# Optimization experiments

Measured on AMD Instinct MI355X. Metric: run time of the kernel, lower is better.

## Reference

```python
import jax, jax.numpy as jnp
import numpy as np

N_QUBITS = 7
N_LAYERS = 2
HILBERT = 2 ** N_QUBITS


def _rx(t):
    c = jnp.cos(t / 2).astype(jnp.complex64)
    s = (-1j * jnp.sin(t / 2)).astype(jnp.complex64)
    return jnp.stack([jnp.stack([c, s]), jnp.stack([s, c])])


def _ry(t):
    c = jnp.cos(t / 2).astype(jnp.complex64)
    s = jnp.sin(t / 2).astype(jnp.complex64)
    return jnp.stack([jnp.stack([c, -s]), jnp.stack([s, c])])


def _rz(t):
    z0 = jnp.exp(-0.5j * t).astype(jnp.complex64)
    z1 = jnp.exp(0.5j * t).astype(jnp.complex64)
    zero = jnp.zeros_like(z0)
    return jnp.stack([jnp.stack([z0, zero]), jnp.stack([zero, z1])])


def _apply_1q(state, U, q):
    # state: [B, 2, 2, ..., 2]; wire q lives on axis q+1 (wire 0 = MSB, PennyLane convention)
    ax = q + 1
    out = jnp.tensordot(U, state, axes=[[1], [ax]])  # new gate axis at 0
    return jnp.moveaxis(out, 0, ax)


def _apply_cnot(state, c, t):
    c_ax, t_ax = c + 1, t + 1
    s0 = jax.lax.index_in_dim(state, 0, c_ax, keepdims=False)
    s1 = jax.lax.index_in_dim(state, 1, c_ax, keepdims=False)
    t2 = t_ax - 1 if t_ax > c_ax else t_ax  # target axis after control axis removed
    s1 = jnp.flip(s1, axis=t2)  # X on target within control=1 block
    return jnp.stack([s0, s1], axis=c_ax)


def setup_inputs() -> dict:
    key = jax.random.key(0)
    k1, k2 = jax.random.split(key)
    x = jax.random.normal(k1, (131072, HILBERT), dtype=jnp.float32)
    weights = jax.random.uniform(k2, (N_LAYERS, N_QUBITS, 3), dtype=jnp.float32) * (2 * np.pi)
    return {"x": x, "weights": weights}


def reference(x, weights):
    B = x.shape[0]
    norms = jnp.maximum(jnp.linalg.norm(x, axis=-1, keepdims=True), 1e-8)
    psi = (x / norms).astype(jnp.complex64)
    state = psi.reshape((B,) + (2,) * N_QUBITS)
    for layer in range(N_LAYERS):
        for q in range(N_QUBITS):
            state = _apply_1q(state, _rx(weights[layer, q, 0]), q)
            state = _apply_1q(state, _ry(weights[layer, q, 1]), q)
            state = _apply_1q(state, _rz(weights[layer, q, 2]), q)
        for q in range(N_QUBITS):
            state = _apply_cnot(state, q, (q + 1) % N_QUBITS)
    probs = jnp.abs(state) ** 2  # real [B, 2,...,2]
    zs = []
    for q in range(N_QUBITS):
        other = tuple(a for a in range(1, N_QUBITS + 1) if a != q + 1)
        p = probs.sum(axis=other)  # [B, 2] marginal of wire q
        zs.append(p[:, 0] - p[:, 1])
    return jnp.stack(zs, axis=-1)  # [B, N_QUBITS]
```

## Files before the change

kernel.cpp:

```cpp
#include <hip/hip_runtime.h>
#include <hip/hip_bf16.h>


typedef __attribute__((ext_vector_type(8)))  short short8;
typedef __attribute__((ext_vector_type(16))) float f32x16;

static __device__ __forceinline__ short f2bf(float f) {
  __bf16 h = (__bf16)f;
  return __builtin_bit_cast(short, h);
}

static __device__ __forceinline__ int widx(int P, int s, int k) {
  return ((((P << 2) + (s >> 5)) * 8 + (k >> 4)) * 64 +
          ((s & 31) + ((k >> 3) & 1) * 32)) * 8 + (k & 7);
}

__global__ void qnn_build_w(const float* __restrict__ wts,
                            short* __restrict__ W) {
  const int k = blockIdx.x;
  const int l = threadIdx.x;

  float c0r = (2 * l     == k) ? 1.f : 0.f, c0i = 0.f;
  float c1r = (2 * l + 1 == k) ? 1.f : 0.f, c1i = 0.f;

  for (int layer = 0; layer < 2; ++layer) {
    for (int q = 0; q < 7; ++q) {
      const float t0 = 0.5f * wts[(layer * 7 + q) * 3 + 0];
      const float t1 = 0.5f * wts[(layer * 7 + q) * 3 + 1];
      const float t2 = 0.5f * wts[(layer * 7 + q) * 3 + 2];
      const float cx = __cosf(t0), sx = __sinf(t0);
      const float cy = __cosf(t1), sy = __sinf(t1);
      const float cz = __cosf(t2), sz = __sinf(t2);
      const float m00r =  cy * cx, m00i =  sy * sx;
      const float m01r = -sy * cx, m01i = -cy * sx;
      const float m10r =  sy * cx, m10i = -cy * sx;
      const float m11r =  cy * cx, m11i = -sy * sx;
      const float g00r = m00r * cz + m00i * sz, g00i = m00i * cz - m00r * sz;
      const float g01r = m01r * cz + m01i * sz, g01i = m01i * cz - m01r * sz;
      const float g10r = m10r * cz - m10i * sz, g10i = m10i * cz + m10r * sz;
      const float g11r = m11r * cz - m11i * sz, g11i = m11i * cz + m11r * sz;

      const int b = 6 - q;
      if (b == 0) {
        const float n0r = g00r*c0r - g00i*c0i + g01r*c1r - g01i*c1i;
        const float n0i = g00r*c0i + g00i*c0r + g01r*c1i + g01i*c1r;
        const float n1r = g10r*c0r - g10i*c0i + g11r*c1r - g11i*c1i;
        const float n1i = g10r*c0i + g10i*c0r + g11r*c1i + g11i*c1r;
        c0r = n0r; c0i = n0i; c1r = n1r; c1i = n1i;
      } else {
        const int xm  = 1 << (b - 1);
        const int myb = (l >> (b - 1)) & 1;
        const float p0r = __shfl_xor(c0r, xm), p0i = __shfl_xor(c0i, xm);
        const float p1r = __shfl_xor(c1r, xm), p1i = __shfl_xor(c1i, xm);
        const float gar = myb ? g11r : g00r, gai = myb ? g11i : g00i;
        const float gbr = myb ? g10r : g01r, gbi = myb ? g10i : g01i;
        const float n0r = gar*c0r - gai*c0i + gbr*p0r - gbi*p0i;
        const float n0i = gar*c0i + gai*c0r + gbr*p0i + gbi*p0r;
        const float n1r = gar*c1r - gai*c1i + gbr*p1r - gbi*p1i;
        const float n1i = gar*c1i + gai*c1r + gbr*p1i + gbi*p1r;
        c0r = n0r; c0i = n0i; c1r = n1r; c1i = n1i;
      }
    }
    #pragma unroll
    for (int q = 0; q < 7; ++q) {
      const int bc = 6 - q;
      const int bt = 6 - ((q + 1) % 7);
      if (bt == 0) {
        if (l & 1) { float tr=c0r, ti=c0i; c0r=c1r; c0i=c1i; c1r=tr; c1i=ti; }
      } else if (bc == 0) {
        c1r = __shfl_xor(c1r, 32);
        c1i = __shfl_xor(c1i, 32);
      } else {
        const int xm = 1 << (bt - 1);
        const float p0r = __shfl_xor(c0r, xm), p0i = __shfl_xor(c0i, xm);
        const float p1r = __shfl_xor(c1r, xm), p1i = __shfl_xor(c1i, xm);
        if ((l >> (bc - 1)) & 1) { c0r=p0r; c0i=p0i; c1r=p1r; c1i=p1i; }
      }
    }
  }

  W[widx(0, 2 * l,     k)] = f2bf(c0r);
  W[widx(0, 2 * l + 1, k)] = f2bf(c1r);
  W[widx(1, 2 * l,     k)] = f2bf(c0i);
  W[widx(1, 2 * l + 1, k)] = f2bf(c1i);
}

__global__ __launch_bounds__(256, 4) void qnn_main(
    const float* __restrict__ x, const short* __restrict__ W,
    float* __restrict__ out) {
  const int tid = threadIdx.x;
  const int l   = tid & 63;
  const int wv  = tid >> 6;
  const int col = l & 31;
  const int h   = l >> 5;

  __shared__ short8 xb[512];
  __shared__ float  red[4][32][7];

  const int t0 = blockIdx.x;

  float4 fa[2], fb[2];
  #pragma unroll
  for (int i = 0; i < 2; ++i) {
    const int p = i * 256 + tid;
    const int r = p >> 4, q = p & 15;
    const float* gp = x + (size_t)(t0 * 32 + r) * 128 + q * 8;
    fa[i] = *reinterpret_cast<const float4*>(gp);
    fb[i] = *reinterpret_cast<const float4*>(gp + 4);
  }

  short8 A0[8], A1[8];
  #pragma unroll
  for (int j = 0; j < 8; ++j) {
    const int off = ((wv * 8 + j) * 64 + l) * 8;
    A0[j] = *reinterpret_cast<const short8*>(W + off);
    A1[j] = *reinterpret_cast<const short8*>(W + 16384 + off);
  }

  #pragma unroll
  for (int i = 0; i < 2; ++i) {
    const int p = i * 256 + tid;
    const int r = p >> 4, q = p & 15;
    short8 c;
    c[0]=f2bf(fa[i].x); c[1]=f2bf(fa[i].y); c[2]=f2bf(fa[i].z); c[3]=f2bf(fa[i].w);
    c[4]=f2bf(fb[i].x); c[5]=f2bf(fb[i].y); c[6]=f2bf(fb[i].z); c[7]=f2bf(fb[i].w);
    xb[r * 16 + (q ^ (r & 7))] = c;
  }
  asm volatile("s_waitcnt lgkmcnt(0)" ::: "memory");
  __builtin_amdgcn_s_barrier();
  asm volatile("" ::: "memory");

  f32x16 acc0 = {0.f,0.f,0.f,0.f,0.f,0.f,0.f,0.f,
                 0.f,0.f,0.f,0.f,0.f,0.f,0.f,0.f};
  f32x16 acc1 = {0.f,0.f,0.f,0.f,0.f,0.f,0.f,0.f,
                 0.f,0.f,0.f,0.f,0.f,0.f,0.f,0.f};
  #pragma unroll
  for (int j = 0; j < 8; ++j) {
    const int q = j * 2 + h;
    const short8 bfr = xb[col * 16 + (q ^ (col & 7))];
    acc0 = __builtin_amdgcn_mfma_f32_32x32x16_bf16(A0[j], bfr, acc0, 0, 0, 0);
    acc1 = __builtin_amdgcn_mfma_f32_32x32x16_bf16(A1[j], bfr, acc1, 0, 0, 0);
  }

  {
    float aS[8], aD[8];
    #pragma unroll
    for (int i = 0; i < 8; ++i) {
      const float pe = acc0[2*i]   * acc0[2*i]   + acc1[2*i]   * acc1[2*i];
      const float po = acc0[2*i+1] * acc0[2*i+1] + acc1[2*i+1] * acc1[2*i+1];
      aS[i] = pe + po;
      aD[i] = pe - po;
    }
    float bS[4], bD[4];
    #pragma unroll
    for (int i = 0; i < 4; ++i) {
      bS[i] = aS[2*i] + aS[2*i+1];
      bD[i] = aS[2*i] - aS[2*i+1];
    }
    float u0 = ((aD[0]+aD[1]) + (aD[2]+aD[3])) + ((aD[4]+aD[5]) + (aD[6]+aD[7]));
    float u1 = (bD[0] + bD[1]) + (bD[2] + bD[3]);
    const float cS0 = bS[0] + bS[1], cD0 = bS[0] - bS[1];
    const float cS1 = bS[2] + bS[3], cD1 = bS[2] - bS[3];
    float u3 = cD0 + cD1;
    float u4 = cS0 - cS1;
    float T  = cS0 + cS1;

    const float Tp = __shfl_xor(T, 32);
    const float u2 = h ? (Tp - T) : (T - Tp);
    T += Tp;
    u0 += __shfl_xor(u0, 32);
    u1 += __shfl_xor(u1, 32);
    u3 += __shfl_xor(u3, 32);
    u4 += __shfl_xor(u4, 32);

    if (h == 0) {
      red[wv][col][0] = T;
      red[wv][col][1] = u0;
      red[wv][col][2] = u1;
      red[wv][col][3] = u2;
      red[wv][col][4] = u3;
      red[wv][col][5] = u4;
    }
  }

  asm volatile("s_waitcnt lgkmcnt(0)" ::: "memory");
  __builtin_amdgcn_s_barrier();
  asm volatile("" ::: "memory");

  if (tid < 32) {
    const int c = tid;
    const float T0 = red[0][c][0], T1 = red[1][c][0];
    const float T2 = red[2][c][0], T3 = red[3][c][0];
    const float sT  = (T0 + T1) + (T2 + T3);
    const float inv = 1.0f / sT;
    const float z0 = (T0 + T1) - (T2 + T3);
    const float z1 = (T0 - T1) + (T2 - T3);
    float zr[5];
    #pragma unroll
    for (int i = 0; i < 5; ++i)
      zr[i] = (red[0][c][5-i] + red[1][c][5-i]) +
              (red[2][c][5-i] + red[3][c][5-i]);
    float* o = out + (size_t)(t0 * 32 + c) * 7;
    o[0] = z0 * inv; o[1] = z1 * inv; o[2] = zr[0] * inv; o[3] = zr[1] * inv;
    o[4] = zr[2] * inv; o[5] = zr[3] * inv; o[6] = zr[4] * inv;
  }
}

extern "C" void kernel_launch(void* const* d_in, const int* in_sizes, int n_in,
                              void* d_out, int out_size, void* d_ws, size_t ws_size,
                              hipStream_t stream) {
  const float* x   = (const float*)d_in[0];
  const float* wts = (const float*)d_in[1];
  float* out = (float*)d_out;
  short* W   = (short*)d_ws;

  const int B     = in_sizes[0] / 128;
  const int grid  = B / 32;

  qnn_build_w<<<128, 64, 0, stream>>>(wts, W);
  qnn_main<<<grid, 256, 0, stream>>>(x, W, out);
}
```

Measured before the change: 25.55 us.

## Process two 32-row tiles per block with double-buffered LDS staging

Each block now handles 64 batch rows as two 32-row halves, so the W fragment loads into registers are amortised over twice as many rows. Global loads for the second half are issued before the first half's MFMA compute and staged into a second LDS buffer afterwards, overlapping memory latency with compute. The grid halves, which reduces parallelism and adds a barrier per stage, and the larger LDS footprint and live registers may lower occupancy.

```diff
diff --git a/kernel.cpp b/kernel.cpp
--- a/kernel.cpp
+++ b/kernel.cpp
@@ -94,20 +94,11 @@
   const int col = l & 31;
   const int h   = l >> 5;
 
-  __shared__ short8 xb[512];
-  __shared__ float  red[4][32][7];
+  __shared__ short8 xb[2][512];
+  __shared__ float  red[4][64][6];
 
   const int t0 = blockIdx.x;
-
-  float4 fa[2], fb[2];
-  #pragma unroll
-  for (int i = 0; i < 2; ++i) {
-    const int p = i * 256 + tid;
-    const int r = p >> 4, q = p & 15;
-    const float* gp = x + (size_t)(t0 * 32 + r) * 128 + q * 8;
-    fa[i] = *reinterpret_cast<const float4*>(gp);
-    fb[i] = *reinterpret_cast<const float4*>(gp + 4);
-  }
+  const float* xbase = x + (size_t)t0 * 64 * 128;
 
   short8 A0[8], A1[8];
   #pragma unroll
@@ -117,32 +108,41 @@
     A1[j] = *reinterpret_cast<const short8*>(W + 16384 + off);
   }
 
-  #pragma unroll
-  for (int i = 0; i < 2; ++i) {
-    const int p = i * 256 + tid;
-    const int r = p >> 4, q = p & 15;
-    short8 c;
-    c[0]=f2bf(fa[i].x); c[1]=f2bf(fa[i].y); c[2]=f2bf(fa[i].z); c[3]=f2bf(fa[i].w);
-    c[4]=f2bf(fb[i].x); c[5]=f2bf(fb[i].y); c[6]=f2bf(fb[i].z); c[7]=f2bf(fb[i].w);
-    xb[r * 16 + (q ^ (r & 7))] = c;
-  }
-  asm volatile("s_waitcnt lgkmcnt(0)" ::: "memory");
-  __builtin_amdgcn_s_barrier();
-  asm volatile("" ::: "memory");
-
-  f32x16 acc0 = {0.f,0.f,0.f,0.f,0.f,0.f,0.f,0.f,
-                 0.f,0.f,0.f,0.f,0.f,0.f,0.f,0.f};
-  f32x16 acc1 = {0.f,0.f,0.f,0.f,0.f,0.f,0.f,0.f,
-                 0.f,0.f,0.f,0.f,0.f,0.f,0.f,0.f};
-  #pragma unroll
-  for (int j = 0; j < 8; ++j) {
-    const int q = j * 2 + h;
-    const short8 bfr = xb[col * 16 + (q ^ (col & 7))];
-    acc0 = __builtin_amdgcn_mfma_f32_32x32x16_bf16(A0[j], bfr, acc0, 0, 0, 0);
-    acc1 = __builtin_amdgcn_mfma_f32_32x32x16_bf16(A1[j], bfr, acc1, 0, 0, 0);
-  }
-
-  {
+  float4 fa[2], fb[2];
+
+  auto LOAD = [&](int H) {
+    #pragma unroll
+    for (int i = 0; i < 2; ++i) {
+      const int p = i * 256 + tid;
+      const int r = p >> 4, q = p & 15;
+      const float* gp = xbase + (size_t)(H * 32 + r) * 128 + q * 8;
+      fa[i] = *reinterpret_cast<const float4*>(gp);
+      fb[i] = *reinterpret_cast<const float4*>(gp + 4);
+    }
+  };
+  auto STAGE = [&](int H) {
+    #pragma unroll
+    for (int i = 0; i < 2; ++i) {
+      const int p = i * 256 + tid;
+      const int r = p >> 4, q = p & 15;
+      short8 c;
+      c[0]=f2bf(fa[i].x); c[1]=f2bf(fa[i].y); c[2]=f2bf(fa[i].z); c[3]=f2bf(fa[i].w);
+      c[4]=f2bf(fb[i].x); c[5]=f2bf(fb[i].y); c[6]=f2bf(fb[i].z); c[7]=f2bf(fb[i].w);
+      xb[H][r * 16 + (q ^ (r & 7))] = c;
+    }
+  };
+  auto COMPUTE = [&](int H) {
+    f32x16 acc0 = {0.f,0.f,0.f,0.f,0.f,0.f,0.f,0.f,
+                   0.f,0.f,0.f,0.f,0.f,0.f,0.f,0.f};
+    f32x16 acc1 = {0.f,0.f,0.f,0.f,0.f,0.f,0.f,0.f,
+                   0.f,0.f,0.f,0.f,0.f,0.f,0.f,0.f};
+    #pragma unroll
+    for (int j = 0; j < 8; ++j) {
+      const int q = j * 2 + h;
+      const short8 bfr = xb[H][col * 16 + (q ^ (col & 7))];
+      acc0 = __builtin_amdgcn_mfma_f32_32x32x16_bf16(A0[j], bfr, acc0, 0, 0, 0);
+      acc1 = __builtin_amdgcn_mfma_f32_32x32x16_bf16(A1[j], bfr, acc1, 0, 0, 0);
+    }
     float aS[8], aD[8];
     #pragma unroll
     for (int i = 0; i < 8; ++i) {
@@ -174,20 +174,36 @@
     u4 += __shfl_xor(u4, 32);
 
     if (h == 0) {
-      red[wv][col][0] = T;
-      red[wv][col][1] = u0;
-      red[wv][col][2] = u1;
-      red[wv][col][3] = u2;
-      red[wv][col][4] = u3;
-      red[wv][col][5] = u4;
-    }
-  }
-
+      const int row = H * 32 + col;
+      red[wv][row][0] = T;
+      red[wv][row][1] = u0;
+      red[wv][row][2] = u1;
+      red[wv][row][3] = u2;
+      red[wv][row][4] = u3;
+      red[wv][row][5] = u4;
+    }
+  };
+
+  LOAD(0);
+  STAGE(0);
+  LOAD(1);
+  asm volatile("" ::: "memory");
   asm volatile("s_waitcnt lgkmcnt(0)" ::: "memory");
   __builtin_amdgcn_s_barrier();
   asm volatile("" ::: "memory");
 
-  if (tid < 32) {
+  COMPUTE(0);
+  STAGE(1);
+  asm volatile("s_waitcnt lgkmcnt(0)" ::: "memory");
+  __builtin_amdgcn_s_barrier();
+  asm volatile("" ::: "memory");
+
+  COMPUTE(1);
+  asm volatile("s_waitcnt lgkmcnt(0)" ::: "memory");
+  __builtin_amdgcn_s_barrier();
+  asm volatile("" ::: "memory");
+
+  if (tid < 64) {
     const int c = tid;
     const float T0 = red[0][c][0], T1 = red[1][c][0];
     const float T2 = red[2][c][0], T3 = red[3][c][0];
@@ -200,7 +216,7 @@
     for (int i = 0; i < 5; ++i)
       zr[i] = (red[0][c][5-i] + red[1][c][5-i]) +
               (red[2][c][5-i] + red[3][c][5-i]);
-    float* o = out + (size_t)(t0 * 32 + c) * 7;
+    float* o = out + (size_t)(t0 * 64 + c) * 7;
     o[0] = z0 * inv; o[1] = z1 * inv; o[2] = zr[0] * inv; o[3] = zr[1] * inv;
     o[4] = zr[2] * inv; o[5] = zr[3] * inv; o[6] = zr[4] * inv;
   }
@@ -215,7 +231,7 @@
   short* W   = (short*)d_ws;
 
   const int B     = in_sizes[0] / 128;
-  const int grid  = B / 32;
+  const int grid  = B / 64;
 
   qnn_build_w<<<128, 64, 0, stream>>>(wts, W);
   qnn_main<<<grid, 256, 0, stream>>>(x, W, out);
```

After: 35.96 us. 40.8% more time.

## Process three batch tiles per block with upfront loads and staged pipeline

Applied to the files above, without the earlier changes.

Each block now handles three 32-row tiles instead of one. All three tiles' global loads are issued up front, then staging, MFMA compute and the output tail are interleaved across tiles with triple-buffered LDS. This amortizes the per-block W fragment load (which stays in registers) and overlaps memory latency with compute. The cost is more registers (launch bounds lowered to 3 waves per SIMD), fewer blocks in the grid, and more LDS per block.

```diff
diff --git a/kernel.cpp b/kernel.cpp
--- a/kernel.cpp
+++ b/kernel.cpp
@@ -85,29 +85,20 @@
   W[widx(1, 2 * l + 1, k)] = f2bf(c1i);
 }
 
-__global__ __launch_bounds__(256, 4) void qnn_main(
+__global__ __launch_bounds__(256, 3) void qnn_main(
     const float* __restrict__ x, const short* __restrict__ W,
-    float* __restrict__ out) {
+    float* __restrict__ out, int ntiles) {
   const int tid = threadIdx.x;
   const int l   = tid & 63;
   const int wv  = tid >> 6;
   const int col = l & 31;
   const int h   = l >> 5;
 
-  __shared__ short8 xb[512];
-  __shared__ float  red[4][32][7];
-
-  const int t0 = blockIdx.x;
-
-  float4 fa[2], fb[2];
-  #pragma unroll
-  for (int i = 0; i < 2; ++i) {
-    const int p = i * 256 + tid;
-    const int r = p >> 4, q = p & 15;
-    const float* gp = x + (size_t)(t0 * 32 + r) * 128 + q * 8;
-    fa[i] = *reinterpret_cast<const float4*>(gp);
-    fb[i] = *reinterpret_cast<const float4*>(gp + 4);
-  }
+  __shared__ short8 xb[3][512];
+  __shared__ float  red[3][4][32][6];
+
+  const int T0 = blockIdx.x * 3;
+  const int NT = min(3, ntiles - T0);
 
   short8 A0[8], A1[8];
   #pragma unroll
@@ -116,33 +107,53 @@
     A0[j] = *reinterpret_cast<const short8*>(W + off);
     A1[j] = *reinterpret_cast<const short8*>(W + 16384 + off);
   }
-
-  #pragma unroll
-  for (int i = 0; i < 2; ++i) {
-    const int p = i * 256 + tid;
-    const int r = p >> 4, q = p & 15;
-    short8 c;
-    c[0]=f2bf(fa[i].x); c[1]=f2bf(fa[i].y); c[2]=f2bf(fa[i].z); c[3]=f2bf(fa[i].w);
-    c[4]=f2bf(fb[i].x); c[5]=f2bf(fb[i].y); c[6]=f2bf(fb[i].z); c[7]=f2bf(fb[i].w);
-    xb[r * 16 + (q ^ (r & 7))] = c;
-  }
-  asm volatile("s_waitcnt lgkmcnt(0)" ::: "memory");
-  __builtin_amdgcn_s_barrier();
-  asm volatile("" ::: "memory");
-
-  f32x16 acc0 = {0.f,0.f,0.f,0.f,0.f,0.f,0.f,0.f,
-                 0.f,0.f,0.f,0.f,0.f,0.f,0.f,0.f};
-  f32x16 acc1 = {0.f,0.f,0.f,0.f,0.f,0.f,0.f,0.f,
-                 0.f,0.f,0.f,0.f,0.f,0.f,0.f,0.f};
-  #pragma unroll
-  for (int j = 0; j < 8; ++j) {
-    const int q = j * 2 + h;
-    const short8 bfr = xb[col * 16 + (q ^ (col & 7))];
-    acc0 = __builtin_amdgcn_mfma_f32_32x32x16_bf16(A0[j], bfr, acc0, 0, 0, 0);
-    acc1 = __builtin_amdgcn_mfma_f32_32x32x16_bf16(A1[j], bfr, acc1, 0, 0, 0);
-  }
-
-  {
+  __builtin_amdgcn_sched_barrier(0);
+
+  float4 s0[4], s1[4], s2[4];
+  auto LOADT = [&](int T, float4* st) {
+    #pragma unroll
+    for (int i = 0; i < 2; ++i) {
+      const int p = i * 256 + tid;
+      const int r = p >> 4, q = p & 15;
+      const float* gp = x + ((size_t)T * 32 + r) * 128 + q * 8;
+      st[2*i]     = *reinterpret_cast<const float4*>(gp);
+      st[2*i + 1] = *reinterpret_cast<const float4*>(gp + 4);
+    }
+  };
+
+  LOADT(T0, s0);
+  __builtin_amdgcn_sched_barrier(0);
+  if (NT > 1) LOADT(T0 + 1, s1);
+  __builtin_amdgcn_sched_barrier(0);
+  if (NT > 2) LOADT(T0 + 2, s2);
+  __builtin_amdgcn_sched_barrier(0);
+
+  auto STAGE = [&](int b, float4* st) {
+    #pragma unroll
+    for (int i = 0; i < 2; ++i) {
+      const int p = i * 256 + tid;
+      const int r = p >> 4, q = p & 15;
+      short8 c;
+      c[0]=f2bf(st[2*i].x);   c[1]=f2bf(st[2*i].y);
+      c[2]=f2bf(st[2*i].z);   c[3]=f2bf(st[2*i].w);
+      c[4]=f2bf(st[2*i+1].x); c[5]=f2bf(st[2*i+1].y);
+      c[6]=f2bf(st[2*i+1].z); c[7]=f2bf(st[2*i+1].w);
+      xb[b][r * 16 + (q ^ (r & 7))] = c;
+    }
+  };
+
+  auto COMPUTE = [&](int b) {
+    f32x16 acc0 = {0.f,0.f,0.f,0.f,0.f,0.f,0.f,0.f,
+                   0.f,0.f,0.f,0.f,0.f,0.f,0.f,0.f};
+    f32x16 acc1 = {0.f,0.f,0.f,0.f,0.f,0.f,0.f,0.f,
+                   0.f,0.f,0.f,0.f,0.f,0.f,0.f,0.f};
+    #pragma unroll
+    for (int j = 0; j < 8; ++j) {
+      const int q = j * 2 + h;
+      const short8 bfr = xb[b][col * 16 + (q ^ (col & 7))];
+      acc0 = __builtin_amdgcn_mfma_f32_32x32x16_bf16(A0[j], bfr, acc0, 0, 0, 0);
+      acc1 = __builtin_amdgcn_mfma_f32_32x32x16_bf16(A1[j], bfr, acc1, 0, 0, 0);
+    }
     float aS[8], aD[8];
     #pragma unroll
     for (int i = 0; i < 8; ++i) {
@@ -174,36 +185,58 @@
     u4 += __shfl_xor(u4, 32);
 
     if (h == 0) {
-      red[wv][col][0] = T;
-      red[wv][col][1] = u0;
-      red[wv][col][2] = u1;
-      red[wv][col][3] = u2;
-      red[wv][col][4] = u3;
-      red[wv][col][5] = u4;
-    }
-  }
-
-  asm volatile("s_waitcnt lgkmcnt(0)" ::: "memory");
-  __builtin_amdgcn_s_barrier();
-  asm volatile("" ::: "memory");
-
-  if (tid < 32) {
-    const int c = tid;
-    const float T0 = red[0][c][0], T1 = red[1][c][0];
-    const float T2 = red[2][c][0], T3 = red[3][c][0];
-    const float sT  = (T0 + T1) + (T2 + T3);
-    const float inv = 1.0f / sT;
-    const float z0 = (T0 + T1) - (T2 + T3);
-    const float z1 = (T0 - T1) + (T2 - T3);
-    float zr[5];
-    #pragma unroll
-    for (int i = 0; i < 5; ++i)
-      zr[i] = (red[0][c][5-i] + red[1][c][5-i]) +
-              (red[2][c][5-i] + red[3][c][5-i]);
-    float* o = out + (size_t)(t0 * 32 + c) * 7;
-    o[0] = z0 * inv; o[1] = z1 * inv; o[2] = zr[0] * inv; o[3] = zr[1] * inv;
-    o[4] = zr[2] * inv; o[5] = zr[3] * inv; o[6] = zr[4] * inv;
-  }
+      red[b][wv][col][0] = T;
+      red[b][wv][col][1] = u0;
+      red[b][wv][col][2] = u1;
+      red[b][wv][col][3] = u2;
+      red[b][wv][col][4] = u3;
+      red[b][wv][col][5] = u4;
+    }
+  };
+
+  auto TAIL = [&](int b, int T) {
+    if (tid < 32) {
+      const int c = tid;
+      const float T0v = red[b][0][c][0], T1v = red[b][1][c][0];
+      const float T2v = red[b][2][c][0], T3v = red[b][3][c][0];
+      const float sT  = (T0v + T1v) + (T2v + T3v);
+      const float inv = 1.0f / sT;
+      const float z0 = (T0v + T1v) - (T2v + T3v);
+      const float z1 = (T0v - T1v) + (T2v - T3v);
+      float zr[5];
+      #pragma unroll
+      for (int i = 0; i < 5; ++i)
+        zr[i] = (red[b][0][c][5-i] + red[b][1][c][5-i]) +
+                (red[b][2][c][5-i] + red[b][3][c][5-i]);
+      float* o = out + (size_t)(T * 32 + c) * 7;
+      o[0] = z0 * inv; o[1] = z1 * inv; o[2] = zr[0] * inv; o[3] = zr[1] * inv;
+      o[4] = zr[2] * inv; o[5] = zr[3] * inv; o[6] = zr[4] * inv;
+    }
+  };
+
+  #define SYNC() do { \
+    asm volatile("s_waitcnt lgkmcnt(0)" ::: "memory"); \
+    __builtin_amdgcn_s_barrier(); \
+    asm volatile("" ::: "memory"); } while (0)
+
+  STAGE(0, s0);
+  SYNC();
+
+  COMPUTE(0);
+  if (NT > 1) STAGE(1, s1);
+  SYNC();
+
+  TAIL(0, T0);
+  if (NT > 1) COMPUTE(1);
+  if (NT > 2) STAGE(2, s2);
+  SYNC();
+
+  if (NT > 1) TAIL(1, T0 + 1);
+  if (NT > 2) COMPUTE(2);
+  SYNC();
+
+  if (NT > 2) TAIL(2, T0 + 2);
+  #undef SYNC
 }
 
 extern "C" void kernel_launch(void* const* d_in, const int* in_sizes, int n_in,
@@ -214,9 +247,10 @@
   float* out = (float*)d_out;
   short* W   = (short*)d_ws;
 
-  const int B     = in_sizes[0] / 128;
-  const int grid  = B / 32;
+  const int B      = in_sizes[0] / 128;
+  const int ntiles = B / 32;
+  const int grid   = (ntiles + 2) / 3;
 
   qnn_build_w<<<128, 64, 0, stream>>>(wts, W);
-  qnn_main<<<grid, 256, 0, stream>>>(x, W, out);
-}
+  qnn_main<<<grid, 256, 0, stream>>>(x, W, out, ntiles);
+}
```

Result: no change. 26.03 us (+1.9%).

## Restructure main kernel: per-wave 32-row tiles with 16x16 MFMA and LDS-staged W

Applied to the files above, without the earlier changes.

The main kernel now launches 512-thread blocks in which each wave handles 32 batch rows on its own. The 128x128 complex unitary is copied once per block into LDS with global_load_lds and read as 16x16x32 bf16 MFMA fragments. Input rows are loaded straight into registers in B-fragment layout, which removes the LDS staging and cross-wave reduction barriers, and the Z-expectation sums are accumulated per output group and combined with wave shuffles. This means fewer, larger blocks that each load the 64KB W into LDS, and more register pressure from 16 float4 input loads per thread.

```diff
diff --git a/kernel.cpp b/kernel.cpp
--- a/kernel.cpp
+++ b/kernel.cpp
@@ -2,17 +2,23 @@
 #include <hip/hip_bf16.h>
 
 
-typedef __attribute__((ext_vector_type(8)))  short short8;
-typedef __attribute__((ext_vector_type(16))) float f32x16;
+typedef __attribute__((ext_vector_type(8))) short short8;
+typedef __attribute__((ext_vector_type(4))) float f32x4;
 
 static __device__ __forceinline__ short f2bf(float f) {
   __bf16 h = (__bf16)f;
   return __builtin_bit_cast(short, h);
 }
 
-static __device__ __forceinline__ int widx(int P, int s, int k) {
-  return ((((P << 2) + (s >> 5)) * 8 + (k >> 4)) * 64 +
-          ((s & 31) + ((k >> 3) & 1) * 32)) * 8 + (k & 7);
+static __device__ __forceinline__ void gl16(const void* g, void* l) {
+  __builtin_amdgcn_global_load_lds(
+      (const __attribute__((address_space(1))) void*)g,
+      (__attribute__((address_space(3))) void*)l, 16, 0, 0);
+}
+
+static __device__ __forceinline__ int widx16(int P, int s, int k) {
+  return (((P * 8 + (s >> 4)) * 4 + (k >> 5)) * 64 +
+          ((s & 15) + 16 * ((k >> 3) & 3))) * 8 + (k & 7);
 }
 
 __global__ void qnn_build_w(const float* __restrict__ wts,
@@ -79,130 +85,158 @@
     }
   }
 
-  W[widx(0, 2 * l,     k)] = f2bf(c0r);
-  W[widx(0, 2 * l + 1, k)] = f2bf(c1r);
-  W[widx(1, 2 * l,     k)] = f2bf(c0i);
-  W[widx(1, 2 * l + 1, k)] = f2bf(c1i);
-}
-
-__global__ __launch_bounds__(256, 4) void qnn_main(
+  W[widx16(0, 2 * l,     k)] = f2bf(c0r);
+  W[widx16(0, 2 * l + 1, k)] = f2bf(c1r);
+  W[widx16(1, 2 * l,     k)] = f2bf(c0i);
+  W[widx16(1, 2 * l + 1, k)] = f2bf(c1i);
+}
+
+__global__ __launch_bounds__(512, 4) void qnn_main(
     const float* __restrict__ x, const short* __restrict__ W,
-    float* __restrict__ out) {
+    float* __restrict__ out, int nrows) {
   const int tid = threadIdx.x;
   const int l   = tid & 63;
   const int wv  = tid >> 6;
-  const int col = l & 31;
-  const int h   = l >> 5;
-
-  __shared__ short8 xb[512];
-  __shared__ float  red[4][32][7];
-
-  const int t0 = blockIdx.x;
-
-  float4 fa[2], fb[2];
-  #pragma unroll
-  for (int i = 0; i < 2; ++i) {
-    const int p = i * 256 + tid;
-    const int r = p >> 4, q = p & 15;
-    const float* gp = x + (size_t)(t0 * 32 + r) * 128 + q * 8;
-    fa[i] = *reinterpret_cast<const float4*>(gp);
-    fb[i] = *reinterpret_cast<const float4*>(gp + 4);
-  }
-
-  short8 A0[8], A1[8];
-  #pragma unroll
-  for (int j = 0; j < 8; ++j) {
-    const int off = ((wv * 8 + j) * 64 + l) * 8;
-    A0[j] = *reinterpret_cast<const short8*>(W + off);
-    A1[j] = *reinterpret_cast<const short8*>(W + 16384 + off);
-  }
-
-  #pragma unroll
-  for (int i = 0; i < 2; ++i) {
-    const int p = i * 256 + tid;
-    const int r = p >> 4, q = p & 15;
-    short8 c;
-    c[0]=f2bf(fa[i].x); c[1]=f2bf(fa[i].y); c[2]=f2bf(fa[i].z); c[3]=f2bf(fa[i].w);
-    c[4]=f2bf(fb[i].x); c[5]=f2bf(fb[i].y); c[6]=f2bf(fb[i].z); c[7]=f2bf(fb[i].w);
-    xb[r * 16 + (q ^ (r & 7))] = c;
-  }
-  asm volatile("s_waitcnt lgkmcnt(0)" ::: "memory");
+  const int q4  = l >> 4;
+  const int r16 = l & 15;
+
+  __shared__ short Wl[32768];
+
+  {
+    const char* gw = (const char*)W;
+    char* lw = (char*)Wl;
+    #pragma unroll
+    for (int i = 0; i < 8; ++i) {
+      const int off = wv * 8192 + i * 1024 + l * 16;
+      gl16(gw + off, lw + off);
+    }
+  }
+  __builtin_amdgcn_sched_barrier(0);
+
+  const int base  = (blockIdx.x * 8 + wv) * 32;
+  const int cbase = (base + 32 <= nrows) ? base : (nrows - 32);
+  float4 xf[16];
+  {
+    const char* gx = (const char*)x + (size_t)cbase * 512;
+    #pragma unroll
+    for (int s = 0; s < 2; ++s)
+      #pragma unroll
+      for (int kf = 0; kf < 4; ++kf) {
+        const int off = (s * 16 + r16) * 512 + kf * 128 + q4 * 32;
+        xf[s * 8 + kf * 2]     = *reinterpret_cast<const float4*>(gx + off);
+        xf[s * 8 + kf * 2 + 1] = *reinterpret_cast<const float4*>(gx + off + 16);
+      }
+  }
+  __builtin_amdgcn_sched_barrier(0);
+
+  asm volatile("s_waitcnt vmcnt(16)" ::: "memory");
   __builtin_amdgcn_s_barrier();
   asm volatile("" ::: "memory");
-
-  f32x16 acc0 = {0.f,0.f,0.f,0.f,0.f,0.f,0.f,0.f,
-                 0.f,0.f,0.f,0.f,0.f,0.f,0.f,0.f};
-  f32x16 acc1 = {0.f,0.f,0.f,0.f,0.f,0.f,0.f,0.f,
-                 0.f,0.f,0.f,0.f,0.f,0.f,0.f,0.f};
+  __builtin_amdgcn_sched_barrier(0);
+
+  short8 bfr0[4], bfr1[4];
   #pragma unroll
-  for (int j = 0; j < 8; ++j) {
-    const int q = j * 2 + h;
-    const short8 bfr = xb[col * 16 + (q ^ (col & 7))];
-    acc0 = __builtin_amdgcn_mfma_f32_32x32x16_bf16(A0[j], bfr, acc0, 0, 0, 0);
-    acc1 = __builtin_amdgcn_mfma_f32_32x32x16_bf16(A1[j], bfr, acc1, 0, 0, 0);
-  }
-
-  {
-    float aS[8], aD[8];
-    #pragma unroll
-    for (int i = 0; i < 8; ++i) {
-      const float pe = acc0[2*i]   * acc0[2*i]   + acc1[2*i]   * acc1[2*i];
-      const float po = acc0[2*i+1] * acc0[2*i+1] + acc1[2*i+1] * acc1[2*i+1];
-      aS[i] = pe + po;
-      aD[i] = pe - po;
-    }
-    float bS[4], bD[4];
-    #pragma unroll
-    for (int i = 0; i < 4; ++i) {
-      bS[i] = aS[2*i] + aS[2*i+1];
-      bD[i] = aS[2*i] - aS[2*i+1];
-    }
-    float u0 = ((aD[0]+aD[1]) + (aD[2]+aD[3])) + ((aD[4]+aD[5]) + (aD[6]+aD[7]));
-    float u1 = (bD[0] + bD[1]) + (bD[2] + bD[3]);
-    const float cS0 = bS[0] + bS[1], cD0 = bS[0] - bS[1];
-    const float cS1 = bS[2] + bS[3], cD1 = bS[2] - bS[3];
-    float u3 = cD0 + cD1;
-    float u4 = cS0 - cS1;
-    float T  = cS0 + cS1;
-
-    const float Tp = __shfl_xor(T, 32);
-    const float u2 = h ? (Tp - T) : (T - Tp);
-    T += Tp;
-    u0 += __shfl_xor(u0, 32);
-    u1 += __shfl_xor(u1, 32);
-    u3 += __shfl_xor(u3, 32);
-    u4 += __shfl_xor(u4, 32);
-
-    if (h == 0) {
-      red[wv][col][0] = T;
-      red[wv][col][1] = u0;
-      red[wv][col][2] = u1;
-      red[wv][col][3] = u2;
-      red[wv][col][4] = u3;
-      red[wv][col][5] = u4;
-    }
-  }
-
-  asm volatile("s_waitcnt lgkmcnt(0)" ::: "memory");
-  __builtin_amdgcn_s_barrier();
-  asm volatile("" ::: "memory");
-
-  if (tid < 32) {
-    const int c = tid;
-    const float T0 = red[0][c][0], T1 = red[1][c][0];
-    const float T2 = red[2][c][0], T3 = red[3][c][0];
-    const float sT  = (T0 + T1) + (T2 + T3);
-    const float inv = 1.0f / sT;
-    const float z0 = (T0 + T1) - (T2 + T3);
-    const float z1 = (T0 - T1) + (T2 - T3);
-    float zr[5];
-    #pragma unroll
-    for (int i = 0; i < 5; ++i)
-      zr[i] = (red[0][c][5-i] + red[1][c][5-i]) +
-              (red[2][c][5-i] + red[3][c][5-i]);
-    float* o = out + (size_t)(t0 * 32 + c) * 7;
-    o[0] = z0 * inv; o[1] = z1 * inv; o[2] = zr[0] * inv; o[3] = zr[1] * inv;
-    o[4] = zr[2] * inv; o[5] = zr[3] * inv; o[6] = zr[4] * inv;
+  for (int kf = 0; kf < 4; ++kf) {
+    const float4 a = xf[kf * 2], b = xf[kf * 2 + 1];
+    short8 c;
+    c[0]=f2bf(a.x); c[1]=f2bf(a.y); c[2]=f2bf(a.z); c[3]=f2bf(a.w);
+    c[4]=f2bf(b.x); c[5]=f2bf(b.y); c[6]=f2bf(b.z); c[7]=f2bf(b.w);
+    bfr0[kf] = c;
+    const float4 d = xf[8 + kf * 2], e = xf[8 + kf * 2 + 1];
+    short8 f;
+    f[0]=f2bf(d.x); f[1]=f2bf(d.y); f[2]=f2bf(d.z); f[3]=f2bf(d.w);
+    f[4]=f2bf(e.x); f[5]=f2bf(e.y); f[6]=f2bf(e.z); f[7]=f2bf(e.w);
+    bfr1[kf] = f;
+  }
+
+  float Tt0 = 0.f, Tt1 = 0.f;
+  float U0[7] = {0.f,0.f,0.f,0.f,0.f,0.f,0.f};
+  float U1[7] = {0.f,0.f,0.f,0.f,0.f,0.f,0.f};
+  const float sg2 = (q4 & 1) ? -1.f : 1.f;
+  const float sg3 = (q4 & 2) ? -1.f : 1.f;
+  const short8* wfrag = reinterpret_cast<const short8*>(Wl);
+
+  #pragma unroll
+  for (int g = 0; g < 8; ++g) {
+    f32x4 a00 = {0.f,0.f,0.f,0.f};
+    f32x4 a10 = {0.f,0.f,0.f,0.f};
+    f32x4 a01 = {0.f,0.f,0.f,0.f};
+    f32x4 a11 = {0.f,0.f,0.f,0.f};
+    #pragma unroll
+    for (int kf = 0; kf < 4; ++kf) {
+      const short8 w0 = wfrag[(g * 4 + kf) * 64 + l];
+      const short8 w1 = wfrag[((8 + g) * 4 + kf) * 64 + l];
+      a00 = __builtin_amdgcn_mfma_f32_16x16x32_bf16(w0, bfr0[kf], a00, 0,0,0);
+      a10 = __builtin_amdgcn_mfma_f32_16x16x32_bf16(w1, bfr0[kf], a10, 0,0,0);
+      a01 = __builtin_amdgcn_mfma_f32_16x16x32_bf16(w0, bfr1[kf], a01, 0,0,0);
+      a11 = __builtin_amdgcn_mfma_f32_16x16x32_bf16(w1, bfr1[kf], a11, 0,0,0);
+    }
+    {
+      const float p0 = a00[0]*a00[0] + a10[0]*a10[0];
+      const float p1 = a00[1]*a00[1] + a10[1]*a10[1];
+      const float p2 = a00[2]*a00[2] + a10[2]*a10[2];
+      const float p3 = a00[3]*a00[3] + a10[3]*a10[3];
+      const float s01 = p0 + p1, s23 = p2 + p3;
+      const float Tg = s01 + s23;
+      U0[0] += (p0 - p1) + (p2 - p3);
+      U0[1] += s01 - s23;
+      U0[2] += sg2 * Tg;
+      U0[3] += sg3 * Tg;
+      U0[4] += (g & 1) ? -Tg : Tg;
+      U0[5] += (g & 2) ? -Tg : Tg;
+      U0[6] += (g & 4) ? -Tg : Tg;
+      Tt0   += Tg;
+    }
+    {
+      const float p0 = a01[0]*a01[0] + a11[0]*a11[0];
+      const float p1 = a01[1]*a01[1] + a11[1]*a11[1];
+      const float p2 = a01[2]*a01[2] + a11[2]*a11[2];
+      const float p3 = a01[3]*a01[3] + a11[3]*a11[3];
+      const float s01 = p0 + p1, s23 = p2 + p3;
+      const float Tg = s01 + s23;
+      U1[0] += (p0 - p1) + (p2 - p3);
+      U1[1] += s01 - s23;
+      U1[2] += sg2 * Tg;
+      U1[3] += sg3 * Tg;
+      U1[4] += (g & 1) ? -Tg : Tg;
+      U1[5] += (g & 2) ? -Tg : Tg;
+      U1[6] += (g & 4) ? -Tg : Tg;
+      Tt1   += Tg;
+    }
+  }
+
+  float v0[8] = {Tt0, U0[0], U0[1], U0[2], U0[3], U0[4], U0[5], U0[6]};
+  float v1[8] = {Tt1, U1[0], U1[1], U1[2], U1[3], U1[4], U1[5], U1[6]};
+  #pragma unroll
+  for (int i = 0; i < 8; ++i) {
+    v0[i] += __shfl_xor(v0[i], 16);
+    v0[i] += __shfl_xor(v0[i], 32);
+    v1[i] += __shfl_xor(v1[i], 16);
+    v1[i] += __shfl_xor(v1[i], 32);
+  }
+
+  if (base < nrows) {
+    if (l < 16) {
+      const float inv = 1.0f / v0[0];
+      float* o = out + (size_t)(base + l) * 7;
+      o[0] = v0[7] * inv;
+      o[1] = v0[6] * inv;
+      o[2] = v0[5] * inv;
+      o[3] = v0[4] * inv;
+      o[4] = v0[3] * inv;
+      o[5] = v0[2] * inv;
+      o[6] = v0[1] * inv;
+    } else if (l < 32) {
+      const float inv = 1.0f / v1[0];
+      float* o = out + (size_t)(base + 16 + (l & 15)) * 7;
+      o[0] = v1[7] * inv;
+      o[1] = v1[6] * inv;
+      o[2] = v1[5] * inv;
+      o[3] = v1[4] * inv;
+      o[4] = v1[3] * inv;
+      o[5] = v1[2] * inv;
+      o[6] = v1[1] * inv;
+    }
   }
 }
 
@@ -214,9 +248,9 @@
   float* out = (float*)d_out;
   short* W   = (short*)d_ws;
 
-  const int B     = in_sizes[0] / 128;
-  const int grid  = B / 32;
+  const int B    = in_sizes[0] / 128;
+  const int grid = (B + 255) / 256;
 
   qnn_build_w<<<128, 64, 0, stream>>>(wts, W);
-  qnn_main<<<grid, 256, 0, stream>>>(x, W, out);
-}
+  qnn_main<<<grid, 512, 0, stream>>>(x, W, out, B);
+}
```

Measured after the change: 35.81 us. 40.2% more time.
